# Optimization experiments

Measured on AMD Instinct MI355X. Metric: run time of the kernel, lower is better.

## Reference

```python
import jax, jax.numpy as jnp
import numpy as np
from jax import lax

N, IN, OUT, R, K = 16384, 128, 128, 3, 16
H = IN  # DGL lstm aggregator: LSTM(in_feats, in_feats)


def setup_inputs() -> dict:
    key = jax.random.key(0)
    ks = jax.random.split(key, 10)
    s_in = np.float32(1.0 / np.sqrt(IN))
    return {
        "x": jax.random.normal(ks[0], (N, IN), jnp.float32),
        "conn": jax.random.normal(ks[1], (N, IN), jnp.float32),
        "nbr_idx": jax.random.randint(ks[2], (R, N, K), 0, N),
        "trans": jax.random.normal(ks[3], (OUT, IN), jnp.float32) * s_in,
        "W_ih": jax.random.normal(ks[4], (R, 4 * H, IN), jnp.float32) * s_in,
        "W_hh": jax.random.normal(ks[5], (R, 4 * H, H), jnp.float32) * s_in,
        "b_lstm": jnp.zeros((R, 4 * H), jnp.float32),
        "fc_self": jax.random.normal(ks[6], (R, OUT, IN), jnp.float32) * s_in,
        "fc_neigh": jax.random.normal(ks[7], (R, OUT, H), jnp.float32) * s_in,
        "bias": jnp.zeros((R, OUT), jnp.float32),
    }


def _lstm_last_hidden(seq, Wih, Whh, b):
    """seq: [N, K, IN] neighbor sequence -> final hidden state [N, H].
    PyTorch/DGL gate order: input, forget, cell, output."""
    n = seq.shape[0]
    h0 = jnp.zeros((n, H), seq.dtype)
    c0 = jnp.zeros((n, H), seq.dtype)

    def step(carry, x_t):
        h, c = carry
        gates = x_t @ Wih.T + h @ Whh.T + b  # [N, 4H]
        i, f, g, o = jnp.split(gates, 4, axis=-1)
        i = jax.nn.sigmoid(i)
        f = jax.nn.sigmoid(f)
        o = jax.nn.sigmoid(o)
        g = jnp.tanh(g)
        c = f * c + i * g
        h = o * jnp.tanh(c)
        return (h, c), None

    (h, _), _ = lax.scan(step, (h0, c0), jnp.swapaxes(seq, 0, 1))  # scan over K
    return h


def reference(x, conn, nbr_idx, trans, W_ih, W_hh, b_lstm, fc_self, fc_neigh, bias):
    outs = []
    for r in range(R):  # small fixed relation set
        nbr = x[nbr_idx[r]]  # [N, K, IN] irregular gather
        h_n = _lstm_last_hidden(nbr, W_ih[r], W_hh[r], b_lstm[r])
        o = x @ fc_self[r].T + h_n @ fc_neigh[r].T + bias[r]
        outs.append(jax.nn.leaky_relu(o))  # slope 0.01 == F.leaky_relu default
    X = jnp.stack(outs, axis=1)  # [N, R, OUT]
    # att_score = (X @ trans) @ conn[:, :, None], softmax over relations
    score = jnp.einsum('nrd,di,ni->nr', X, trans, conn)
    att = jax.nn.softmax(score, axis=1)
    return jnp.einsum('nrd,nr->nd', X, att)  # [N, OUT]
```

## Files before the change

kernel.cpp:

```cpp
#include <hip/hip_runtime.h>

#define NN    16384
#define HD    128
#define G4    512
#define KST   16
#define NRELS 3
#define NPB   16

using f16x8 = __attribute__((ext_vector_type(8))) _Float16;
using f32x4 = __attribute__((ext_vector_type(4))) float;

static __device__ __forceinline__ f32x4 f4splat(float v) {
    f32x4 r; r[0] = v; r[1] = v; r[2] = v; r[3] = v; return r;
}
static __device__ __forceinline__ f16x8 load8h(const float* p) {
    const float4 a = ((const float4*)p)[0];
    const float4 b = ((const float4*)p)[1];
    f16x8 r;
    r[0] = (_Float16)a.x; r[1] = (_Float16)a.y; r[2] = (_Float16)a.z; r[3] = (_Float16)a.w;
    r[4] = (_Float16)b.x; r[5] = (_Float16)b.y; r[6] = (_Float16)b.z; r[7] = (_Float16)b.w;
    return r;
}
static __device__ __forceinline__ f32x4 mfma16h(f16x8 a, f16x8 b, f32x4 c) {
    return __builtin_amdgcn_mfma_f32_16x16x32_f16(a, b, c, 0, 0, 0);
}
static __device__ __forceinline__ unsigned short f2h_bits(float f) {
    return __builtin_bit_cast(unsigned short, (_Float16)f);
}
static __device__ __forceinline__ float h2f(unsigned short b) {
    return (float)__builtin_bit_cast(_Float16, b);
}
static __device__ __forceinline__ float sigm(float x) {
    return __builtin_amdgcn_rcpf(1.0f + __expf(-x));
}
static __device__ __forceinline__ float tanh_(float x) {
    return 2.0f * __builtin_amdgcn_rcpf(1.0f + __expf(-2.0f * x)) - 1.0f;
}
static __device__ __forceinline__ void barrier_lgkm() {
    asm volatile("s_waitcnt lgkmcnt(0)" ::: "memory");
    __builtin_amdgcn_s_barrier();
}

template <int OUTC, int MODE>
__global__ __launch_bounds__(512, 2) void gemm_rt(
    const float* __restrict__ A, const float* __restrict__ W,
    const float* __restrict__ bias, void* __restrict__ outp)
{
    constexpr int CW = OUTC / 8;
    constexpr int CT = CW / 16;
    const int tid = threadIdx.x;
    const int w = tid >> 6, lane = tid & 63;
    const int g = lane >> 4, m = lane & 15;
    const int n0 = blockIdx.x * 64;
    const int r = blockIdx.y;
    const float* Wr = W + (size_t)r * OUTC * HD;

    f32x4 acc[4][CT];
#pragma unroll
    for (int rt = 0; rt < 4; ++rt)
#pragma unroll
        for (int ct = 0; ct < CT; ++ct) acc[rt][ct] = f4splat(0.0f);

#pragma unroll
    for (int kc = 0; kc < 4; ++kc) {
        f16x8 a[4];
#pragma unroll
        for (int rt = 0; rt < 4; ++rt)
            a[rt] = load8h(A + (size_t)(n0 + rt * 16 + m) * HD + kc * 32 + 8 * g);
        f16x8 b[CT];
#pragma unroll
        for (int ct = 0; ct < CT; ++ct)
            b[ct] = load8h(Wr + (size_t)(w * CW + ct * 16 + m) * HD + kc * 32 + 8 * g);
#pragma unroll
        for (int rt = 0; rt < 4; ++rt)
#pragma unroll
            for (int ct = 0; ct < CT; ++ct)
                acc[rt][ct] = mfma16h(a[rt], b[ct], acc[rt][ct]);
    }

#pragma unroll
    for (int rt = 0; rt < 4; ++rt)
#pragma unroll
        for (int ct = 0; ct < CT; ++ct) {
            const int col = w * CW + ct * 16 + m;
            const float bv = bias ? bias[r * OUTC + col] : 0.0f;
#pragma unroll
            for (int e = 0; e < 4; ++e) {
                const int row = n0 + rt * 16 + 4 * g + e;
                const float v = acc[rt][ct][e] + bv;
                if constexpr (MODE == 0) {
                    ((float*)outp)[(size_t)row * OUTC + col] = v;
                } else {
                    ((unsigned short*)outp)[((size_t)r * NN + row) * G4 + (size_t)(col & 127) * 4 + (col >> 7)] =
                        f2h_bits(v);
                }
            }
        }
}

__global__ __launch_bounds__(512, 4) void lstm_kernel(
    const float* __restrict__ x, const int* __restrict__ nbr,
    const float* __restrict__ Whh, const float* __restrict__ fcs,
    const float* __restrict__ fcn, const float* __restrict__ bias,
    const unsigned short* __restrict__ xW, float* __restrict__ Xout)
{
    __shared__ unsigned short h_lds[2][NPB * HD];
    __shared__ int idx_lds[KST * NPB];

    const int tid = threadIdx.x;
    const int w = tid >> 6, lane = tid & 63;
    const int g = lane >> 4, m = lane & 15;
    const int n0 = blockIdx.x * NPB;
    const int r = blockIdx.y;
    const unsigned laneoff = (unsigned)(w * 16 + m) * 8u;
    const char* xwr = (const char*)(xW + (size_t)r * NN * G4);

    if (tid < KST * NPB) {
        const int t = tid >> 4, n = tid & 15;
        idx_lds[tid] = nbr[((size_t)r * NN + n0 + n) * KST + t] << 10;
    }

    f16x8 bw[4][4];
    const float* whr = Whh + (size_t)r * G4 * HD;
#pragma unroll
    for (int q = 0; q < 4; ++q)
#pragma unroll
        for (int kc = 0; kc < 4; ++kc)
            bw[q][kc] = load8h(whr + (size_t)(q * 128 + w * 16 + m) * HD + kc * 32 + 8 * g);

    int rd_off[4], wr_off[4];
#pragma unroll
    for (int kc = 0; kc < 4; ++kc)
        rd_off[kc] = m * HD + ((kc * 32 + 8 * g) ^ ((m & 7) << 3));
#pragma unroll
    for (int e = 0; e < 4; ++e) {
        const int row = 4 * g + e;
        wr_off[e] = row * HD + ((w * 16 + m) ^ ((row & 7) << 3));
    }

    float cst[4] = {0.0f, 0.0f, 0.0f, 0.0f};
    barrier_lgkm();

    ushort4 xv[4];
    {
        const int4 i4 = *(const int4*)&idx_lds[4 * g];
        xv[0] = *(const ushort4*)(xwr + (unsigned)i4.x + laneoff);
        xv[1] = *(const ushort4*)(xwr + (unsigned)i4.y + laneoff);
        xv[2] = *(const ushort4*)(xwr + (unsigned)i4.z + laneoff);
        xv[3] = *(const ushort4*)(xwr + (unsigned)i4.w + laneoff);
    }

    int cur = 0;
    for (int t = 0; t < KST; ++t) {
        f32x4 acc[4];
#pragma unroll
        for (int e = 0; e < 4; ++e) {
            acc[0][e] = h2f(xv[e].x);
            acc[1][e] = h2f(xv[e].y);
            acc[2][e] = h2f(xv[e].z);
            acc[3][e] = h2f(xv[e].w);
        }

        if (t + 1 < KST) {
            const int4 i4 = *(const int4*)&idx_lds[(t + 1) * 16 + 4 * g];
            xv[0] = *(const ushort4*)(xwr + (unsigned)i4.x + laneoff);
            xv[1] = *(const ushort4*)(xwr + (unsigned)i4.y + laneoff);
            xv[2] = *(const ushort4*)(xwr + (unsigned)i4.z + laneoff);
            xv[3] = *(const ushort4*)(xwr + (unsigned)i4.w + laneoff);
        }

        if (t > 0) {
            const unsigned short* hb = h_lds[cur];
#pragma unroll
            for (int kc = 0; kc < 4; ++kc) {
                const f16x8 a = *(const f16x8*)&hb[rd_off[kc]];
#pragma unroll
                for (int q = 0; q < 4; ++q)
                    acc[q] = mfma16h(a, bw[q][kc], acc[q]);
            }
        }

        unsigned short* nh = h_lds[cur ^ 1];
#pragma unroll
        for (int e = 0; e < 4; ++e) {
            const float iv = sigm(acc[0][e]);
            const float fv = sigm(acc[1][e]);
            const float gv = tanh_(acc[2][e]);
            const float ov = sigm(acc[3][e]);
            const float cn = fv * cst[e] + iv * gv;
            cst[e] = cn;
            nh[wr_off[e]] = f2h_bits(ov * tanh_(cn));
        }
        barrier_lgkm();
        cur ^= 1;
    }

    {
        const unsigned short* hb = h_lds[cur];
        const float* fsr = fcs + (size_t)r * HD * HD;
        const float* fnr = fcn + (size_t)r * HD * HD;
        const int col = w * 16 + m;
        f32x4 oacc = f4splat(bias[r * HD + col]);
#pragma unroll
        for (int kc = 0; kc < 4; ++kc) {
            const f16x8 ax = load8h(x + (size_t)(n0 + m) * HD + kc * 32 + 8 * g);
            const f16x8 ah = *(const f16x8*)&hb[rd_off[kc]];
            const f16x8 bs = load8h(fsr + (size_t)col * HD + kc * 32 + 8 * g);
            const f16x8 bn = load8h(fnr + (size_t)col * HD + kc * 32 + 8 * g);
            oacc = mfma16h(ax, bs, oacc);
            oacc = mfma16h(ah, bn, oacc);
        }
#pragma unroll
        for (int e = 0; e < 4; ++e) {
            const int row = 4 * g + e;
            float v = oacc[e];
            v = v > 0.0f ? v : 0.01f * v;
            Xout[((size_t)(n0 + row) * NRELS + r) * HD + col] = v;
        }
    }
}

__global__ __launch_bounds__(256) void attn_kernel(
    const float* __restrict__ X, const float* __restrict__ tc,
    float* __restrict__ out)
{
    const int wv = blockIdx.x * (blockDim.x >> 6) + (threadIdx.x >> 6);
    const int lane = threadIdx.x & 63;
    if (wv >= NN) return;
    const size_t nb = (size_t)wv;

    const float t0 = tc[nb * HD + lane];
    const float t1 = tc[nb * HD + 64 + lane];
    float x0[3], x1[3], sc[3];
#pragma unroll
    for (int r = 0; r < 3; ++r) {
        x0[r] = X[(nb * 3 + r) * HD + lane];
        x1[r] = X[(nb * 3 + r) * HD + 64 + lane];
        float p = x0[r] * t0 + x1[r] * t1;
#pragma unroll
        for (int off = 32; off >= 1; off >>= 1)
            p += __shfl_xor(p, off, 64);
        sc[r] = p;
    }
    const float mx = fmaxf(sc[0], fmaxf(sc[1], sc[2]));
    const float e0 = __expf(sc[0] - mx), e1 = __expf(sc[1] - mx), e2 = __expf(sc[2] - mx);
    const float inv = __builtin_amdgcn_rcpf(e0 + e1 + e2);
    const float a0 = e0 * inv, a1 = e1 * inv, a2 = e2 * inv;
    out[nb * HD + lane]      = a0 * x0[0] + a1 * x0[1] + a2 * x0[2];
    out[nb * HD + 64 + lane] = a0 * x1[0] + a1 * x1[1] + a2 * x1[2];
}

extern "C" void kernel_launch(void* const* d_in, const int* in_sizes, int n_in,
                              void* d_out, int out_size, void* d_ws, size_t ws_size,
                              hipStream_t stream)
{
    const float* x     = (const float*)d_in[0];
    const float* conn  = (const float*)d_in[1];
    const int*   nbr   = (const int*)d_in[2];
    const float* trans = (const float*)d_in[3];
    const float* Wih   = (const float*)d_in[4];
    const float* Whh   = (const float*)d_in[5];
    const float* blstm = (const float*)d_in[6];
    const float* fcs   = (const float*)d_in[7];
    const float* fcn   = (const float*)d_in[8];
    const float* bias  = (const float*)d_in[9];
    float* out = (float*)d_out;

    const size_t XW_B = (size_t)NRELS * NN * G4 * 2;
    const size_t TC_B = (size_t)NN * HD * 4;
    const size_t XO_B = (size_t)NN * NRELS * HD * 4;
    if (ws_size < XW_B + TC_B + XO_B) return;

    char* wsb = (char*)d_ws;
    unsigned short* xW = (unsigned short*)wsb;
    float*          tc = (float*)(wsb + XW_B);
    float*          Xo = (float*)(wsb + XW_B + TC_B);

    gemm_rt<512, 1><<<dim3(NN / 64, NRELS), 512, 0, stream>>>(x, Wih, blstm, (void*)xW);
    gemm_rt<128, 0><<<dim3(NN / 64, 1), 512, 0, stream>>>(conn, trans, nullptr, (void*)tc);
    lstm_kernel<<<dim3(NN / NPB, NRELS), 512, 0, stream>>>(x, nbr, Whh, fcs, fcn, bias, xW, Xo);
    attn_kernel<<<dim3(NN / 4), 256, 0, stream>>>(Xo, tc, out);
}
```

Before: 333.5 us.

## Split LSTM gate GEMM across two wave groups with LDS exchange

The LSTM recurrence kernel now uses 1024 threads per block. Two groups of eight waves each compute half of the four gate blocks, so each wave holds only two gate weight fragments instead of four. The second group passes its g/o gate results to the first through LDS as packed fp16, and the first group applies the nonlinearities and writes h in an MFMA-fragment layout. The aim is to cut per-step MFMA latency and register pressure on the serial time loop. In exchange it adds a second barrier per step, an extra LDS round trip, and fp16 rounding of the g/o gate pre-activations.

```diff
diff --git a/kernel.cpp b/kernel.cpp
--- a/kernel.cpp
+++ b/kernel.cpp
@@ -98,113 +98,116 @@
         }
 }
 
-__global__ __launch_bounds__(512, 4) void lstm_kernel(
+__global__ __launch_bounds__(1024, 8) void lstm_kernel(
     const float* __restrict__ x, const int* __restrict__ nbr,
     const float* __restrict__ Whh, const float* __restrict__ fcs,
     const float* __restrict__ fcn, const float* __restrict__ bias,
     const unsigned short* __restrict__ xW, float* __restrict__ Xout)
 {
-    __shared__ unsigned short h_lds[2][NPB * HD];
+    __shared__ char h_fr[2][4096];
+    __shared__ char gx[8192];
     __shared__ int idx_lds[KST * NPB];
 
     const int tid = threadIdx.x;
-    const int w = tid >> 6, lane = tid & 63;
+    const int W = tid >> 6, lane = tid & 63;
     const int g = lane >> 4, m = lane & 15;
+    const int qp = W >> 3, ct = W & 7;
     const int n0 = blockIdx.x * NPB;
     const int r = blockIdx.y;
-    const unsigned laneoff = (unsigned)(w * 16 + m) * 8u;
-    const char* xwr = (const char*)(xW + (size_t)r * NN * G4);
 
     if (tid < KST * NPB) {
         const int t = tid >> 4, n = tid & 15;
         idx_lds[tid] = nbr[((size_t)r * NN + n0 + n) * KST + t] << 10;
     }
 
-    f16x8 bw[4][4];
+    f16x8 bw[2][4];
     const float* whr = Whh + (size_t)r * G4 * HD;
 #pragma unroll
-    for (int q = 0; q < 4; ++q)
+    for (int j = 0; j < 2; ++j)
 #pragma unroll
         for (int kc = 0; kc < 4; ++kc)
-            bw[q][kc] = load8h(whr + (size_t)(q * 128 + w * 16 + m) * HD + kc * 32 + 8 * g);
-
-    int rd_off[4], wr_off[4];
-#pragma unroll
-    for (int kc = 0; kc < 4; ++kc)
-        rd_off[kc] = m * HD + ((kc * 32 + 8 * g) ^ ((m & 7) << 3));
-#pragma unroll
-    for (int e = 0; e < 4; ++e) {
-        const int row = 4 * g + e;
-        wr_off[e] = row * HD + ((w * 16 + m) ^ ((row & 7) << 3));
-    }
-
-    float cst[4] = {0.0f, 0.0f, 0.0f, 0.0f};
-    barrier_lgkm();
-
-    ushort4 xv[4];
-    {
+            bw[j][kc] = load8h(whr + (size_t)((2 * qp + j) * 128 + ct * 16 + m) * HD + kc * 32 + 8 * g);
+
+    const int rd_base = lane << 4;
+    const int gx_addr = ((ct << 6) | lane) << 4;
+    const int col = ct * 16 + m;
+    const int hw_base = ((col >> 5) << 10) + (((col >> 3) & 3) << 8) + (g << 6) + ((col & 7) << 1);
+    const unsigned laneoff = (unsigned)col << 3;
+    const char* xwr = (const char*)(xW + (size_t)r * NN * G4);
+
+    float cst[4] = {0.f, 0.f, 0.f, 0.f};
+    ushort4 xva[4], xvb[4];
+
+    __syncthreads();
+
+    if (qp == 0) {
         const int4 i4 = *(const int4*)&idx_lds[4 * g];
-        xv[0] = *(const ushort4*)(xwr + (unsigned)i4.x + laneoff);
-        xv[1] = *(const ushort4*)(xwr + (unsigned)i4.y + laneoff);
-        xv[2] = *(const ushort4*)(xwr + (unsigned)i4.z + laneoff);
-        xv[3] = *(const ushort4*)(xwr + (unsigned)i4.w + laneoff);
-    }
-
-    int cur = 0;
+        xva[0] = *(const ushort4*)(xwr + (unsigned)i4.x + laneoff);
+        xva[1] = *(const ushort4*)(xwr + (unsigned)i4.y + laneoff);
+        xva[2] = *(const ushort4*)(xwr + (unsigned)i4.z + laneoff);
+        xva[3] = *(const ushort4*)(xwr + (unsigned)i4.w + laneoff);
+    }
+
+#pragma unroll
     for (int t = 0; t < KST; ++t) {
-        f32x4 acc[4];
-#pragma unroll
-        for (int e = 0; e < 4; ++e) {
-            acc[0][e] = h2f(xv[e].x);
-            acc[1][e] = h2f(xv[e].y);
-            acc[2][e] = h2f(xv[e].z);
-            acc[3][e] = h2f(xv[e].w);
-        }
-
-        if (t + 1 < KST) {
+        const int RB = t & 1;
+        const int WB = RB ^ 1;
+        ushort4 (&xv_cur)[4] = (t & 1) ? xvb : xva;
+        ushort4 (&xv_nxt)[4] = (t & 1) ? xva : xvb;
+
+        f32x4 acc0 = f4splat(0.f), acc1 = f4splat(0.f);
+        if (t > 0) {
+#pragma unroll
+            for (int kc = 0; kc < 4; ++kc) {
+                const f16x8 a = *(const f16x8*)(h_fr[RB] + kc * 1024 + rd_base);
+                acc0 = mfma16h(a, bw[0][kc], acc0);
+                acc1 = mfma16h(a, bw[1][kc], acc1);
+            }
+        }
+        if (qp == 0 && t + 1 < KST) {
             const int4 i4 = *(const int4*)&idx_lds[(t + 1) * 16 + 4 * g];
-            xv[0] = *(const ushort4*)(xwr + (unsigned)i4.x + laneoff);
-            xv[1] = *(const ushort4*)(xwr + (unsigned)i4.y + laneoff);
-            xv[2] = *(const ushort4*)(xwr + (unsigned)i4.z + laneoff);
-            xv[3] = *(const ushort4*)(xwr + (unsigned)i4.w + laneoff);
-        }
-
-        if (t > 0) {
-            const unsigned short* hb = h_lds[cur];
-#pragma unroll
-            for (int kc = 0; kc < 4; ++kc) {
-                const f16x8 a = *(const f16x8*)&hb[rd_off[kc]];
-#pragma unroll
-                for (int q = 0; q < 4; ++q)
-                    acc[q] = mfma16h(a, bw[q][kc], acc[q]);
-            }
-        }
-
-        unsigned short* nh = h_lds[cur ^ 1];
-#pragma unroll
-        for (int e = 0; e < 4; ++e) {
-            const float iv = sigm(acc[0][e]);
-            const float fv = sigm(acc[1][e]);
-            const float gv = tanh_(acc[2][e]);
-            const float ov = sigm(acc[3][e]);
-            const float cn = fv * cst[e] + iv * gv;
-            cst[e] = cn;
-            nh[wr_off[e]] = f2h_bits(ov * tanh_(cn));
+            xv_nxt[0] = *(const ushort4*)(xwr + (unsigned)i4.x + laneoff);
+            xv_nxt[1] = *(const ushort4*)(xwr + (unsigned)i4.y + laneoff);
+            xv_nxt[2] = *(const ushort4*)(xwr + (unsigned)i4.z + laneoff);
+            xv_nxt[3] = *(const ushort4*)(xwr + (unsigned)i4.w + laneoff);
+        }
+        if (qp == 1) {
+            f16x8 p;
+#pragma unroll
+            for (int e = 0; e < 4; ++e) {
+                p[2 * e]     = (_Float16)acc0[e];
+                p[2 * e + 1] = (_Float16)acc1[e];
+            }
+            *(f16x8*)(gx + gx_addr) = p;
         }
         barrier_lgkm();
-        cur ^= 1;
-    }
-
-    {
-        const unsigned short* hb = h_lds[cur];
+
+        if (qp == 0) {
+            const f16x8 pg = *(const f16x8*)(gx + gx_addr);
+#pragma unroll
+            for (int e = 0; e < 4; ++e) {
+                const float gi = acc0[e] + h2f(xv_cur[e].x);
+                const float gf = acc1[e] + h2f(xv_cur[e].y);
+                const float gg = (float)pg[2 * e]     + h2f(xv_cur[e].z);
+                const float go = (float)pg[2 * e + 1] + h2f(xv_cur[e].w);
+                const float iv = sigm(gi), fv = sigm(gf);
+                const float gv = tanh_(gg), ov = sigm(go);
+                const float cn = fv * cst[e] + iv * gv;
+                cst[e] = cn;
+                *(unsigned short*)(h_fr[WB] + hw_base + e * 16) = f2h_bits(ov * tanh_(cn));
+            }
+        }
+        barrier_lgkm();
+    }
+
+    if (qp == 0) {
         const float* fsr = fcs + (size_t)r * HD * HD;
         const float* fnr = fcn + (size_t)r * HD * HD;
-        const int col = w * 16 + m;
         f32x4 oacc = f4splat(bias[r * HD + col]);
 #pragma unroll
         for (int kc = 0; kc < 4; ++kc) {
             const f16x8 ax = load8h(x + (size_t)(n0 + m) * HD + kc * 32 + 8 * g);
-            const f16x8 ah = *(const f16x8*)&hb[rd_off[kc]];
+            const f16x8 ah = *(const f16x8*)(h_fr[0] + kc * 1024 + rd_base);
             const f16x8 bs = load8h(fsr + (size_t)col * HD + kc * 32 + 8 * g);
             const f16x8 bn = load8h(fnr + (size_t)col * HD + kc * 32 + 8 * g);
             oacc = mfma16h(ax, bs, oacc);
@@ -278,6 +281,6 @@
 
     gemm_rt<512, 1><<<dim3(NN / 64, NRELS), 512, 0, stream>>>(x, Wih, blstm, (void*)xW);
     gemm_rt<128, 0><<<dim3(NN / 64, 1), 512, 0, stream>>>(conn, trans, nullptr, (void*)tc);
-    lstm_kernel<<<dim3(NN / NPB, NRELS), 512, 0, stream>>>(x, nbr, Whh, fcs, fcn, bias, xW, Xo);
+    lstm_kernel<<<dim3(NN / NPB, NRELS), 1024, 0, stream>>>(x, nbr, Whh, fcs, fcn, bias, xW, Xo);
     attn_kernel<<<dim3(NN / 4), 256, 0, stream>>>(Xo, tc, out);
 }
```

Result: slower. 978.6 us (+193.5%).

## Stage gathered input projections through LDS with coalesced row loads, double-buffered

Applied to the files above, without the earlier changes.

Replaces the per-lane scattered 8-byte gathers of precomputed input-gate rows with whole-row 16-byte-per-lane coalesced loads. Each wave fetches two neighbor rows, writes them into a double-buffered LDS tile, and the fragments are then read from LDS. Loads are issued two steps ahead, and MFMA sections get raised wave priority. This adds 32KB of LDS per block, which may lower occupancy under the 4-blocks launch bound. The final h buffer index is hardcoded to 0, which is correct only because KST is even.

```diff
diff --git a/kernel.cpp b/kernel.cpp
--- a/kernel.cpp
+++ b/kernel.cpp
@@ -105,6 +105,7 @@
     const unsigned short* __restrict__ xW, float* __restrict__ Xout)
 {
     __shared__ unsigned short h_lds[2][NPB * HD];
+    __shared__ unsigned short xbuf[2][NPB * G4];
     __shared__ int idx_lds[KST * NPB];
 
     const int tid = threadIdx.x;
@@ -112,7 +113,6 @@
     const int g = lane >> 4, m = lane & 15;
     const int n0 = blockIdx.x * NPB;
     const int r = blockIdx.y;
-    const unsigned laneoff = (unsigned)(w * 16 + m) * 8u;
     const char* xwr = (const char*)(xW + (size_t)r * NN * G4);
 
     if (tid < KST * NPB) {
@@ -137,21 +137,37 @@
         const int row = 4 * g + e;
         wr_off[e] = row * HD + ((w * 16 + m) ^ ((row & 7) << 3));
     }
+    const int xb_wrA = (2 * w) * G4 + lane * 8;
+    const int xb_wrB = (2 * w + 1) * G4 + lane * 8;
+    const int xb_rd  = (4 * g) * G4 + (w * 16 + m) * 4;
 
     float cst[4] = {0.0f, 0.0f, 0.0f, 0.0f};
+    __syncthreads();
+
+    uint4 pa, pb;
+    {
+        const unsigned oa = (unsigned)idx_lds[0 * 16 + 2 * w];
+        const unsigned ob = (unsigned)idx_lds[0 * 16 + 2 * w + 1];
+        pa = *(const uint4*)(xwr + oa + lane * 16);
+        pb = *(const uint4*)(xwr + ob + lane * 16);
+        *(uint4*)&xbuf[0][xb_wrA] = pa;
+        *(uint4*)&xbuf[0][xb_wrB] = pb;
+        const unsigned oa1 = (unsigned)idx_lds[1 * 16 + 2 * w];
+        const unsigned ob1 = (unsigned)idx_lds[1 * 16 + 2 * w + 1];
+        pa = *(const uint4*)(xwr + oa1 + lane * 16);
+        pb = *(const uint4*)(xwr + ob1 + lane * 16);
+    }
     barrier_lgkm();
 
-    ushort4 xv[4];
-    {
-        const int4 i4 = *(const int4*)&idx_lds[4 * g];
-        xv[0] = *(const ushort4*)(xwr + (unsigned)i4.x + laneoff);
-        xv[1] = *(const ushort4*)(xwr + (unsigned)i4.y + laneoff);
-        xv[2] = *(const ushort4*)(xwr + (unsigned)i4.z + laneoff);
-        xv[3] = *(const ushort4*)(xwr + (unsigned)i4.w + laneoff);
-    }
-
-    int cur = 0;
     for (int t = 0; t < KST; ++t) {
+        const int rb = t & 1;
+        const int wb = rb ^ 1;
+
+        ushort4 xv[4];
+#pragma unroll
+        for (int e = 0; e < 4; ++e)
+            xv[e] = *(const ushort4*)&xbuf[rb][xb_rd + e * G4];
+
         f32x4 acc[4];
 #pragma unroll
         for (int e = 0; e < 4; ++e) {
@@ -161,16 +177,9 @@
             acc[3][e] = h2f(xv[e].w);
         }
 
-        if (t + 1 < KST) {
-            const int4 i4 = *(const int4*)&idx_lds[(t + 1) * 16 + 4 * g];
-            xv[0] = *(const ushort4*)(xwr + (unsigned)i4.x + laneoff);
-            xv[1] = *(const ushort4*)(xwr + (unsigned)i4.y + laneoff);
-            xv[2] = *(const ushort4*)(xwr + (unsigned)i4.z + laneoff);
-            xv[3] = *(const ushort4*)(xwr + (unsigned)i4.w + laneoff);
-        }
-
+        __builtin_amdgcn_s_setprio(1);
         if (t > 0) {
-            const unsigned short* hb = h_lds[cur];
+            const unsigned short* hb = h_lds[rb];
 #pragma unroll
             for (int kc = 0; kc < 4; ++kc) {
                 const f16x8 a = *(const f16x8*)&hb[rd_off[kc]];
@@ -179,8 +188,20 @@
                     acc[q] = mfma16h(a, bw[q][kc], acc[q]);
             }
         }
-
-        unsigned short* nh = h_lds[cur ^ 1];
+        __builtin_amdgcn_s_setprio(0);
+
+        if (t + 1 < KST) {
+            *(uint4*)&xbuf[wb][xb_wrA] = pa;
+            *(uint4*)&xbuf[wb][xb_wrB] = pb;
+            if (t + 2 < KST) {
+                const unsigned oa = (unsigned)idx_lds[(t + 2) * 16 + 2 * w];
+                const unsigned ob = (unsigned)idx_lds[(t + 2) * 16 + 2 * w + 1];
+                pa = *(const uint4*)(xwr + oa + lane * 16);
+                pb = *(const uint4*)(xwr + ob + lane * 16);
+            }
+        }
+
+        unsigned short* nh = h_lds[wb];
 #pragma unroll
         for (int e = 0; e < 4; ++e) {
             const float iv = sigm(acc[0][e]);
@@ -192,11 +213,10 @@
             nh[wr_off[e]] = f2h_bits(ov * tanh_(cn));
         }
         barrier_lgkm();
-        cur ^= 1;
     }
 
     {
-        const unsigned short* hb = h_lds[cur];
+        const unsigned short* hb = h_lds[KST & 1 ? 0 : 0];
         const float* fsr = fcs + (size_t)r * HD * HD;
         const float* fnr = fcn + (size_t)r * HD * HD;
         const int col = w * 16 + m;
```

Result: faster. 325.6 us (-2.4%).

## Process 32 nodes per LSTM block with two row tiles sharing W_hh registers

Applied to the files above, without the earlier changes.

Doubles the number of nodes per block from 16 to 32. Each wave now runs two 16-row MFMA tiles per timestep against the same register-resident W_hh fragments, which amortizes the weight loads and the per-step barrier over twice the work and gives the scheduler more independent MFMAs. It also raises wave priority around the MFMA section with s_setprio. In exchange it doubles the accumulator and gather registers per thread, which may lower occupancy under the 512x4 launch bounds, and it halves the grid size.

```diff
diff --git a/kernel.cpp b/kernel.cpp
--- a/kernel.cpp
+++ b/kernel.cpp
@@ -5,7 +5,7 @@
 #define G4    512
 #define KST   16
 #define NRELS 3
-#define NPB   16
+#define NPB   32
 
 using f16x8 = __attribute__((ext_vector_type(8))) _Float16;
 using f32x4 = __attribute__((ext_vector_type(4))) float;
@@ -115,8 +115,8 @@
     const unsigned laneoff = (unsigned)(w * 16 + m) * 8u;
     const char* xwr = (const char*)(xW + (size_t)r * NN * G4);
 
-    if (tid < KST * NPB) {
-        const int t = tid >> 4, n = tid & 15;
+    {
+        const int t = tid >> 5, n = tid & 31;
         idx_lds[tid] = nbr[((size_t)r * NN + n0 + n) * KST + t] << 10;
     }
 
@@ -138,85 +138,106 @@
         wr_off[e] = row * HD + ((w * 16 + m) ^ ((row & 7) << 3));
     }
 
-    float cst[4] = {0.0f, 0.0f, 0.0f, 0.0f};
-    barrier_lgkm();
-
-    ushort4 xv[4];
+    float cst[2][4] = {{0.f, 0.f, 0.f, 0.f}, {0.f, 0.f, 0.f, 0.f}};
+    __syncthreads();
+
+    ushort4 xv[2][4];
+#pragma unroll
+    for (int rt = 0; rt < 2; ++rt) {
+        const int4 i4 = *(const int4*)&idx_lds[rt * 16 + 4 * g];
+        xv[rt][0] = *(const ushort4*)(xwr + (unsigned)i4.x + laneoff);
+        xv[rt][1] = *(const ushort4*)(xwr + (unsigned)i4.y + laneoff);
+        xv[rt][2] = *(const ushort4*)(xwr + (unsigned)i4.z + laneoff);
+        xv[rt][3] = *(const ushort4*)(xwr + (unsigned)i4.w + laneoff);
+    }
+
+    for (int t = 0; t < KST; ++t) {
+        const int rb = t & 1;
+        const int wb = rb ^ 1;
+
+        f32x4 acc[2][4];
+#pragma unroll
+        for (int rt = 0; rt < 2; ++rt)
+#pragma unroll
+            for (int e = 0; e < 4; ++e) {
+                acc[rt][0][e] = h2f(xv[rt][e].x);
+                acc[rt][1][e] = h2f(xv[rt][e].y);
+                acc[rt][2][e] = h2f(xv[rt][e].z);
+                acc[rt][3][e] = h2f(xv[rt][e].w);
+            }
+
+        if (t + 1 < KST) {
+#pragma unroll
+            for (int rt = 0; rt < 2; ++rt) {
+                const int4 i4 = *(const int4*)&idx_lds[(t + 1) * 32 + rt * 16 + 4 * g];
+                xv[rt][0] = *(const ushort4*)(xwr + (unsigned)i4.x + laneoff);
+                xv[rt][1] = *(const ushort4*)(xwr + (unsigned)i4.y + laneoff);
+                xv[rt][2] = *(const ushort4*)(xwr + (unsigned)i4.z + laneoff);
+                xv[rt][3] = *(const ushort4*)(xwr + (unsigned)i4.w + laneoff);
+            }
+        }
+
+        __builtin_amdgcn_s_setprio(1);
+        if (t > 0) {
+            const unsigned short* hb = h_lds[rb];
+#pragma unroll
+            for (int kc = 0; kc < 4; ++kc) {
+#pragma unroll
+                for (int rt = 0; rt < 2; ++rt) {
+                    const f16x8 a = *(const f16x8*)&hb[rd_off[kc] + rt * 2048];
+#pragma unroll
+                    for (int q = 0; q < 4; ++q)
+                        acc[rt][q] = mfma16h(a, bw[q][kc], acc[rt][q]);
+                }
+            }
+        }
+        __builtin_amdgcn_s_setprio(0);
+
+        unsigned short* nh = h_lds[wb];
+#pragma unroll
+        for (int rt = 0; rt < 2; ++rt)
+#pragma unroll
+            for (int e = 0; e < 4; ++e) {
+                const float iv = sigm(acc[rt][0][e]);
+                const float fv = sigm(acc[rt][1][e]);
+                const float gv = tanh_(acc[rt][2][e]);
+                const float ov = sigm(acc[rt][3][e]);
+                const float cn = fv * cst[rt][e] + iv * gv;
+                cst[rt][e] = cn;
+                nh[wr_off[e] + rt * 2048] = f2h_bits(ov * tanh_(cn));
+            }
+        barrier_lgkm();
+    }
+
     {
-        const int4 i4 = *(const int4*)&idx_lds[4 * g];
-        xv[0] = *(const ushort4*)(xwr + (unsigned)i4.x + laneoff);
-        xv[1] = *(const ushort4*)(xwr + (unsigned)i4.y + laneoff);
-        xv[2] = *(const ushort4*)(xwr + (unsigned)i4.z + laneoff);
-        xv[3] = *(const ushort4*)(xwr + (unsigned)i4.w + laneoff);
-    }
-
-    int cur = 0;
-    for (int t = 0; t < KST; ++t) {
-        f32x4 acc[4];
-#pragma unroll
-        for (int e = 0; e < 4; ++e) {
-            acc[0][e] = h2f(xv[e].x);
-            acc[1][e] = h2f(xv[e].y);
-            acc[2][e] = h2f(xv[e].z);
-            acc[3][e] = h2f(xv[e].w);
-        }
-
-        if (t + 1 < KST) {
-            const int4 i4 = *(const int4*)&idx_lds[(t + 1) * 16 + 4 * g];
-            xv[0] = *(const ushort4*)(xwr + (unsigned)i4.x + laneoff);
-            xv[1] = *(const ushort4*)(xwr + (unsigned)i4.y + laneoff);
-            xv[2] = *(const ushort4*)(xwr + (unsigned)i4.z + laneoff);
-            xv[3] = *(const ushort4*)(xwr + (unsigned)i4.w + laneoff);
-        }
-
-        if (t > 0) {
-            const unsigned short* hb = h_lds[cur];
-#pragma unroll
-            for (int kc = 0; kc < 4; ++kc) {
-                const f16x8 a = *(const f16x8*)&hb[rd_off[kc]];
-#pragma unroll
-                for (int q = 0; q < 4; ++q)
-                    acc[q] = mfma16h(a, bw[q][kc], acc[q]);
-            }
-        }
-
-        unsigned short* nh = h_lds[cur ^ 1];
-#pragma unroll
-        for (int e = 0; e < 4; ++e) {
-            const float iv = sigm(acc[0][e]);
-            const float fv = sigm(acc[1][e]);
-            const float gv = tanh_(acc[2][e]);
-            const float ov = sigm(acc[3][e]);
-            const float cn = fv * cst[e] + iv * gv;
-            cst[e] = cn;
-            nh[wr_off[e]] = f2h_bits(ov * tanh_(cn));
-        }
-        barrier_lgkm();
-        cur ^= 1;
-    }
-
-    {
-        const unsigned short* hb = h_lds[cur];
+        const unsigned short* hb = h_lds[0];
         const float* fsr = fcs + (size_t)r * HD * HD;
         const float* fnr = fcn + (size_t)r * HD * HD;
         const int col = w * 16 + m;
-        f32x4 oacc = f4splat(bias[r * HD + col]);
+        f32x4 oacc[2];
+        oacc[0] = f4splat(bias[r * HD + col]);
+        oacc[1] = oacc[0];
 #pragma unroll
         for (int kc = 0; kc < 4; ++kc) {
-            const f16x8 ax = load8h(x + (size_t)(n0 + m) * HD + kc * 32 + 8 * g);
-            const f16x8 ah = *(const f16x8*)&hb[rd_off[kc]];
             const f16x8 bs = load8h(fsr + (size_t)col * HD + kc * 32 + 8 * g);
             const f16x8 bn = load8h(fnr + (size_t)col * HD + kc * 32 + 8 * g);
-            oacc = mfma16h(ax, bs, oacc);
-            oacc = mfma16h(ah, bn, oacc);
+#pragma unroll
+            for (int rt = 0; rt < 2; ++rt) {
+                const f16x8 ax = load8h(x + (size_t)(n0 + rt * 16 + m) * HD + kc * 32 + 8 * g);
+                const f16x8 ah = *(const f16x8*)&hb[rd_off[kc] + rt * 2048];
+                oacc[rt] = mfma16h(ax, bs, oacc[rt]);
+                oacc[rt] = mfma16h(ah, bn, oacc[rt]);
+            }
         }
 #pragma unroll
-        for (int e = 0; e < 4; ++e) {
-            const int row = 4 * g + e;
-            float v = oacc[e];
-            v = v > 0.0f ? v : 0.01f * v;
-            Xout[((size_t)(n0 + row) * NRELS + r) * HD + col] = v;
-        }
+        for (int rt = 0; rt < 2; ++rt)
+#pragma unroll
+            for (int e = 0; e < 4; ++e) {
+                const int row = rt * 16 + 4 * g + e;
+                float v = oacc[rt][e];
+                v = v > 0.0f ? v : 0.01f * v;
+                Xout[((size_t)(n0 + row) * NRELS + r) * HD + col] = v;
+            }
     }
 }
 
```

Measured after the change: 429.6 us. 28.8% more time.
